# Performance work log

Measured on AMD Instinct MI355X. Metric: run time of the kernel, lower is better.

The kernel has to match this reference:

```python
import jax, jax.numpy as jnp
import numpy as np

DIM = 128
SUPPORT = 1
NL, NM, NG = 5, 20, 100
EPS_BN = 1e-5
EPS_NORM = 1e-12


def knn_idx(vertices, k):
    # vertices: (b, v, 3) -> (b, v, k) indices of k nearest (excluding self)
    sq = jnp.sum(vertices * vertices, axis=-1)  # (b, v)
    dist = -2.0 * jnp.einsum('bic,bjc->bij', vertices, vertices) + sq[:, :, None] + sq[:, None, :]
    _, idx = jax.lax.top_k(-dist, k + 1)  # smallest distances
    return idx[:, :, 1:]


def gather_nbr(t, idx):
    # t: (b, v, c), idx: (b, v, n) -> (b, v, n, c)
    b = t.shape[0]
    return t[jnp.arange(b)[:, None, None], idx]


def conv_layer(idx, vertices, fmap, W, bias, dirs):
    # idx: (b,v,n); fmap: (b,v,DIM); W: (DIM,(S+1)*DIM); bias: ((S+1)*DIM,); dirs: (3,S*DIM)
    nbrs = gather_nbr(vertices, idx)                      # (b,v,n,3)
    d = nbrs - vertices[:, :, None, :]
    d = d / jnp.maximum(jnp.linalg.norm(d, axis=-1, keepdims=True), EPS_NORM)
    sd = dirs / jnp.maximum(jnp.linalg.norm(dirs, axis=0, keepdims=True), EPS_NORM)
    theta = jax.nn.relu(jnp.einsum('bvnc,ck->bvnk', d, sd))  # (b,v,n,S*DIM)
    fo = fmap @ W + bias                                   # (b,v,(S+1)*DIM)
    center = fo[..., :DIM]
    supp = gather_nbr(fo[..., DIM:], idx)                  # (b,v,n,S*DIM)
    b_, v_, n_ = idx.shape
    act = (theta * supp).reshape(b_, v_, n_, SUPPORT, DIM)
    act = jnp.max(act, axis=2).sum(axis=2)                 # max over neighbors, sum over supports
    return center + act                                    # (b,v,DIM)


def bn_relu(x, gamma, beta):
    # training-mode BatchNorm1d over (batch, points) per channel, then ReLU
    mu = jnp.mean(x, axis=(0, 1))
    var = jnp.var(x, axis=(0, 1))
    return jax.nn.relu((x - mu) * jax.lax.rsqrt(var + EPS_BN) * gamma + beta)


def setup_inputs() -> dict:
    key = jax.random.key(0)
    ks = jax.random.split(key, 8)
    B, V = 2, 1024
    return {
        'vertices': jax.random.normal(ks[0], (B, V, 3), jnp.float32),
        'x': jax.random.normal(ks[1], (B, V, DIM), jnp.float32),
        'conv_W': jax.random.normal(ks[2], (6, DIM, (SUPPORT + 1) * DIM), jnp.float32) * 0.05,
        'conv_b': jax.random.normal(ks[3], (6, (SUPPORT + 1) * DIM), jnp.float32) * 0.05,
        'conv_dirs': jax.random.normal(ks[4], (6, 3, SUPPORT * DIM), jnp.float32),
        'bn_gamma': jnp.ones((6, DIM), jnp.float32),
        'bn_beta': jnp.zeros((6, DIM), jnp.float32),
        'down_W': jax.random.normal(ks[5], (3 * DIM, 2 * DIM), jnp.float32) * 0.05,
        'down_b': jax.random.normal(ks[6], (2 * DIM,), jnp.float32) * 0.05,
    }


def reference(vertices, x, conv_W, conv_b, conv_dirs, bn_gamma, bn_beta, down_W, down_b):
    il = knn_idx(vertices, NL)
    im = knn_idx(vertices, NM)
    ig = knn_idx(vertices, NG)
    # param index order: 0=l, 1=m0, 2=m1, 3=g0, 4=g1, 5=g2 (g2 unused, per source bug)
    fl = bn_relu(conv_layer(il, vertices, x, conv_W[0], conv_b[0], conv_dirs[0]), bn_gamma[0], bn_beta[0])
    fm = bn_relu(conv_layer(im, vertices, x, conv_W[1], conv_b[1], conv_dirs[1]), bn_gamma[1], bn_beta[1])
    fm = bn_relu(conv_layer(im, vertices, fm, conv_W[2], conv_b[2], conv_dirs[2]), bn_gamma[2], bn_beta[2])
    fg = bn_relu(conv_layer(ig, vertices, x, conv_W[3], conv_b[3], conv_dirs[3]), bn_gamma[3], bn_beta[3])
    fg = bn_relu(conv_layer(ig, vertices, fg, conv_W[4], conv_b[4], conv_dirs[4]), bn_gamma[4], bn_beta[4])
    # source reuses conv_g0 / bn_g0 for the third global layer
    fg = bn_relu(conv_layer(ig, vertices, fg, conv_W[3], conv_b[3], conv_dirs[3]), bn_gamma[3], bn_beta[3])
    out = jnp.concatenate([fl, fm, fg], axis=2)            # (b, v, 3*DIM)
    return jax.nn.relu(out @ down_W + down_b)              # (b, v, 2*DIM)
```

## Files before the change

### kernel.cpp

```cpp
#include <hip/hip_runtime.h>

__device__ __forceinline__ void do_gemm(
    const float* __restrict__ in, const float* __restrict__ st,
    const float* __restrict__ gm, const float* __restrict__ bt,
    const float* __restrict__ W, const float* __restrict__ bi,
    float* __restrict__ out, int rb, char* smemc)
{
    float* rows  = (float*)smemc;
    float* wch   = rows + 1024;
    float* scale = wch + 4096;
    float* shift = scale + 128;
    int t = threadIdx.x;
    if (t < 128) {
        float sc = 1.0f, sf = 0.0f;
        if (st) {
            float mu  = st[t] * (1.0f/2048.0f);
            float var = st[128+t] * (1.0f/2048.0f) - mu*mu;
            sc = rsqrtf(var + 1e-5f) * gm[t];
            sf = bt[t] - mu*sc;
        }
        scale[t] = sc; shift[t] = sf;
    }
    __syncthreads();
    int r0 = rb * 8;
    {
        float4 v = ((const float4*)(in + r0*128))[t];
        if (st) {
            int c4 = (t & 31) << 2;
            v.x = fmaxf(v.x*scale[c4  ] + shift[c4  ], 0.0f);
            v.y = fmaxf(v.y*scale[c4+1] + shift[c4+1], 0.0f);
            v.z = fmaxf(v.z*scale[c4+2] + shift[c4+2], 0.0f);
            v.w = fmaxf(v.w*scale[c4+3] + shift[c4+3], 0.0f);
        }
        ((float4*)rows)[t] = v;
    }
    int cb = t & 63, rp = (t >> 6) << 1;
    const float* a0r = rows + rp*128;
    const float* a1r = a0r + 128;
    const float4* W4 = (const float4*)W;
    float4* wch4 = (float4*)wch;
    float4 acc0 = make_float4(0.f,0.f,0.f,0.f);
    float4 acc1 = make_float4(0.f,0.f,0.f,0.f);
    for (int c = 0; c < 8; ++c) {
        __syncthreads();
        #pragma unroll
        for (int i = 0; i < 4; ++i)
            wch4[t + 256*i] = W4[c*1024 + t + 256*i];
        __syncthreads();
        int kb = c*16;
        #pragma unroll
        for (int k = 0; k < 16; k += 4) {
            float4 a0 = *(const float4*)(a0r + kb + k);
            float4 a1 = *(const float4*)(a1r + kb + k);
            float4 w;
            w = wch4[(k+0)*64+cb];
            acc0.x += a0.x*w.x; acc0.y += a0.x*w.y; acc0.z += a0.x*w.z; acc0.w += a0.x*w.w;
            acc1.x += a1.x*w.x; acc1.y += a1.x*w.y; acc1.z += a1.x*w.z; acc1.w += a1.x*w.w;
            w = wch4[(k+1)*64+cb];
            acc0.x += a0.y*w.x; acc0.y += a0.y*w.y; acc0.z += a0.y*w.z; acc0.w += a0.y*w.w;
            acc1.x += a1.y*w.x; acc1.y += a1.y*w.y; acc1.z += a1.y*w.z; acc1.w += a1.y*w.w;
            w = wch4[(k+2)*64+cb];
            acc0.x += a0.z*w.x; acc0.y += a0.z*w.y; acc0.z += a0.z*w.z; acc0.w += a0.z*w.w;
            acc1.x += a1.z*w.x; acc1.y += a1.z*w.y; acc1.z += a1.z*w.z; acc1.w += a1.z*w.w;
            w = wch4[(k+3)*64+cb];
            acc0.x += a0.w*w.x; acc0.y += a0.w*w.y; acc0.z += a0.w*w.z; acc0.w += a0.w*w.w;
            acc1.x += a1.w*w.x; acc1.y += a1.w*w.y; acc1.z += a1.w*w.z; acc1.w += a1.w*w.w;
        }
    }
    float4 b4 = ((const float4*)bi)[cb];
    acc0.x += b4.x; acc0.y += b4.y; acc0.z += b4.z; acc0.w += b4.w;
    acc1.x += b4.x; acc1.y += b4.y; acc1.z += b4.z; acc1.w += b4.w;
    ((float4*)out)[(r0+rp  )*64 + cb] = acc0;
    ((float4*)out)[(r0+rp+1)*64 + cb] = acc1;
}

__global__ void k1_kernel(const float* __restrict__ verts, const float* __restrict__ dirs,
                          const float* __restrict__ x,
                          const float* __restrict__ convW, const float* __restrict__ convB,
                          int* __restrict__ idxout, float* __restrict__ sdn,
                          float* __restrict__ st, float* __restrict__ fo)
{
    __shared__ __align__(16) char smem[21504];
    int t = threadIdx.x;
    int blk = blockIdx.x;

    if (blk >= 1280) {
        if (blk == 1286) {
            for (int i = t; i < 768; i += 256) {
                int l = i >> 7, k = i & 127;
                float a = dirs[l*384 + k];
                float b = dirs[l*384 + 128 + k];
                float c = dirs[l*384 + 256 + k];
                float nrm = sqrtf(a*a + b*b + c*c);
                float inv = 1.0f / fmaxf(nrm, 1e-12f);
                sdn[l*384 + k]       = a*inv;
                sdn[l*384 + 128 + k] = b*inv;
                sdn[l*384 + 256 + k] = c*inv;
            }
        } else {
            st[(blk - 1280)*256 + t] = 0.0f;
        }
        return;
    }
    if (blk >= 512) {
        int g = blk - 512;
        int s = g >> 8, rb = g & 255;
        int wi = (s==0) ? 0 : (s==1) ? 1 : 3;
        do_gemm(x, (const float*)0, (const float*)0, (const float*)0,
                convW + wi*32768, convB + wi*256, fo + s*524288, rb, smem);
        return;
    }

    float* xs  = (float*)smem;
    float* ys  = xs + 1024;
    float* zs  = ys + 1024;
    float* sqs = zs + 1024;
    unsigned int* histBase = (unsigned int*)(smem + 16384);
    unsigned int* selBase  = (unsigned int*)(smem + 20480);

    int w = t >> 6, l = t & 63;
    int vglob = blk*4 + w;
    int b = vglob >> 10;
    int v = vglob & 1023;
    unsigned long long* keys = (unsigned long long*)smem + w*256;
    unsigned int* hist = histBase + w*256;
    unsigned int* sel  = selBase + w*4;

    const float* vb = verts + b * 3072;
    for (int i = t; i < 1024; i += 256) {
        float xx = vb[i*3+0], yy = vb[i*3+1], zz = vb[i*3+2];
        xs[i] = xx; ys[i] = yy; zs[i] = zz;
        sqs[i] = xx*xx + yy*yy + zz*zz;
    }
    __syncthreads();

    float cx = xs[v], cy = ys[v], cz = zs[v], csq = sqs[v];
    unsigned long long K16[16];
    #pragma unroll
    for (int q = 0; q < 16; ++q) {
        int j = q*64 + l;
        float dot = cx*xs[j] + cy*ys[j] + cz*zs[j];
        float d = -2.0f*dot + csq + sqs[j];
        unsigned int u = __float_as_uint(d);
        u = (u & 0x80000000u) ? ~u : (u | 0x80000000u);
        K16[q] = (((unsigned long long)u) << 32) | (unsigned long long)j;
    }
    #pragma unroll
    for (int i = 0; i < 4; ++i) hist[l*4 + i] = 0u;
    __syncthreads();

    #pragma unroll
    for (int q = 0; q < 16; ++q)
        atomicAdd(&hist[(unsigned int)(K16[q] >> 56)], 1u);
    __syncthreads();

    {
        unsigned int h0 = hist[l*4], h1 = hist[l*4+1], h2 = hist[l*4+2], h3 = hist[l*4+3];
        unsigned int c1 = h0, c2 = h0+h1, c3 = h0+h1+h2, T = c3+h3;
        unsigned int xacc = T;
        #pragma unroll
        for (int off = 1; off < 64; off <<= 1) {
            unsigned int y = __shfl_up(xacc, off, 64);
            if (l >= off) xacc += y;
        }
        unsigned int P = xacc - T;
        unsigned int ex[4] = {P, P+c1, P+c2, P+c3};
        unsigned int hh[4] = {h0, h1, h2, h3};
        #pragma unroll
        for (int i = 0; i < 4; ++i) {
            if (ex[i] < 101u && ex[i] + hh[i] >= 101u) {
                sel[0] = (unsigned int)(l*4 + i);
                sel[1] = 101u - ex[i];
            }
        }
    }
    __syncthreads();
    unsigned int P8 = sel[0], rank2 = sel[1];
    #pragma unroll
    for (int i = 0; i < 4; ++i) hist[l*4 + i] = 0u;
    __syncthreads();

    #pragma unroll
    for (int q = 0; q < 16; ++q)
        if ((unsigned int)(K16[q] >> 56) == P8)
            atomicAdd(&hist[(unsigned int)(K16[q] >> 48) & 0xFFu], 1u);
    __syncthreads();

    {
        unsigned int h0 = hist[l*4], h1 = hist[l*4+1], h2 = hist[l*4+2], h3 = hist[l*4+3];
        unsigned int c1 = h0, c2 = h0+h1, c3 = h0+h1+h2, T = c3+h3;
        unsigned int xacc = T;
        #pragma unroll
        for (int off = 1; off < 64; off <<= 1) {
            unsigned int y = __shfl_up(xacc, off, 64);
            if (l >= off) xacc += y;
        }
        unsigned int P = xacc - T;
        unsigned int ex[4] = {P, P+c1, P+c2, P+c3};
        unsigned int hh[4] = {h0, h1, h2, h3};
        #pragma unroll
        for (int i = 0; i < 4; ++i) {
            if (ex[i] < rank2 && ex[i] + hh[i] >= rank2) {
                sel[2] = (P8 << 8) | (unsigned int)(l*4 + i);
                sel[3] = 0u;
            }
        }
    }
    __syncthreads();
    unsigned int P16 = sel[2];

    #pragma unroll
    for (int q = 0; q < 16; ++q) {
        if ((unsigned int)(K16[q] >> 48) <= P16) {
            unsigned int pos = atomicAdd(&sel[3], 1u);
            if (pos < 256u) keys[pos] = K16[q];
        }
    }
    __syncthreads();
    unsigned int cnt = sel[3];

    unsigned long long K[4];
    #pragma unroll
    for (int q = 0; q < 4; ++q) {
        unsigned int e = (unsigned int)(l*4 + q);
        K[q] = (e < cnt) ? keys[e] : 0xFFFFFFFFFFFFFFFFULL;
    }

    auto cswap = [&](int qa, int qb, int k) {
        int e = (l << 2) + qa;
        bool up = ((e & k) == 0);
        unsigned long long a = K[qa], bb2 = K[qb];
        unsigned long long mn = a < bb2 ? a : bb2;
        unsigned long long mx = a < bb2 ? bb2 : a;
        K[qa] = up ? mn : mx;
        K[qb] = up ? mx : mn;
    };
    #pragma unroll
    for (int k = 2; k <= 256; k <<= 1) {
        for (int j = k >> 1; j >= 4; j >>= 1) {
            int lj = j >> 2;
            #pragma unroll
            for (int q = 0; q < 4; ++q) {
                unsigned long long other = __shfl_xor(K[q], lj, 64);
                int e = (l << 2) + q;
                bool up = ((e & k) == 0);
                bool lower = ((l & lj) == 0);
                bool takeMin = (lower == up);
                unsigned long long mn = K[q] < other ? K[q] : other;
                unsigned long long mx = K[q] < other ? other : K[q];
                K[q] = takeMin ? mn : mx;
            }
        }
        if (k >= 4) { cswap(0, 2, k); cswap(1, 3, k); }
        cswap(0, 1, k); cswap(2, 3, k);
    }

    #pragma unroll
    for (int q = 0; q < 4; ++q) {
        int e = l*4 + q;
        if (e >= 1 && e <= 100)
            idxout[vglob*100 + (e-1)] = (int)(K[q] & 0xFFFFFFFFu);
    }
}

__global__ void agg_kernel(const int* __restrict__ idx, const float* __restrict__ verts,
                           const float* __restrict__ sdn, const float* __restrict__ fo,
                           int n0, int n1, int n2, int d0, int d1, int d2,
                           float* o0, float* o1, float* o2)
{
    __shared__ float4 ds4s[200];
    __shared__ int jss[200];
    int slot = blockIdx.y;
    int n  = slot==0 ? n0 : slot==1 ? n1 : n2;
    int dI = slot==0 ? d0 : slot==1 ? d1 : d2;
    float* outp = slot==0 ? o0 : slot==1 ? o1 : o2;
    const float* fos = fo + slot * 524288;
    const float* sd = sdn + dI * 384;

    int t = threadIdx.x;
    int h = t >> 7, tt = t & 127;
    float4* ds4 = ds4s + h*100;
    int* js = jss + h*100;
    int r = blockIdx.x*2 + h;
    int b = r >> 10;

    if (tt < n) {
        int j = idx[r*100 + tt];
        js[tt] = j;
        const float* pj = verts + (b*1024 + j)*3;
        const float* pv = verts + r*3;
        float dx = pj[0]-pv[0], dy = pj[1]-pv[1], dz = pj[2]-pv[2];
        float nm = sqrtf(dx*dx + dy*dy + dz*dz);
        float inv = 1.0f / fmaxf(nm, 1e-12f);
        ds4[tt] = make_float4(dx*inv, dy*inv, dz*inv, 0.0f);
    }
    __syncthreads();
    float s0 = sd[tt], s1 = sd[128+tt], s2 = sd[256+tt];
    int bb = b * 1024;
    float m = -3.0e38f;
    for (int q = 0; q < n; q += 5) {
        float th[5];
        const float* p[5];
        #pragma unroll
        for (int u = 0; u < 5; ++u) {
            float4 dq = ds4[q+u];
            th[u] = fmaxf(dq.x*s0 + dq.y*s1 + dq.z*s2, 0.0f);
            p[u] = fos + (size_t)(bb + js[q+u])*256 + 128 + tt;
        }
        float vv[5];
        #pragma unroll
        for (int u = 0; u < 5; ++u) vv[u] = *p[u];
        #pragma unroll
        for (int u = 0; u < 5; ++u) m = fmaxf(m, th[u]*vv[u]);
    }
    outp[r*128 + tt] = fos[r*256 + tt] + m;
}

__global__ void stats_kernel(const float* p0, const float* p1, const float* p2,
                             int i0, int i1, int i2, float* stats)
{
    int slot = blockIdx.y;
    const float* p = slot==0 ? p0 : slot==1 ? p1 : p2;
    float* st = stats + (slot==0 ? i0 : slot==1 ? i1 : i2) * 256;
    __shared__ float s1[256], s2[256];
    int t = threadIdx.x, k = t & 127, half = t >> 7;
    int r0 = blockIdx.x * 128;
    float sum = 0.0f, sq = 0.0f;
    for (int s = 0; s < 64; ++s) {
        float x = p[(r0 + half + 2*s)*128 + k];
        sum += x; sq += x*x;
    }
    s1[t] = sum; s2[t] = sq;
    __syncthreads();
    if (t < 128) {
        atomicAdd(&st[k],     s1[t] + s1[t+128]);
        atomicAdd(&st[128+k], s2[t] + s2[t+128]);
    }
}

__global__ void gemm2_kernel(
    const float* inA, const float* stA, const float* gA, const float* beA,
    const float* WA, const float* biA, float* foA,
    const float* inB, const float* stB, const float* gB, const float* beB,
    const float* WB, const float* biB, float* foB)
{
    __shared__ __align__(16) char smem[21504];
    if (blockIdx.y == 0)
        do_gemm(inA, stA, gA, beA, WA, biA, foA, blockIdx.x, smem);
    else
        do_gemm(inB, stB, gB, beB, WB, biB, foB, blockIdx.x, smem);
}

__global__ void down_kernel(
    const float* __restrict__ p0, const float* __restrict__ st0,
    const float* __restrict__ g0, const float* __restrict__ be0,
    const float* __restrict__ p1, const float* __restrict__ st1,
    const float* __restrict__ g1, const float* __restrict__ be1,
    const float* __restrict__ p2, const float* __restrict__ st2,
    const float* __restrict__ g2, const float* __restrict__ be2,
    const float* __restrict__ dW, const float* __restrict__ db,
    float* __restrict__ out)
{
    __shared__ float rows[8*384];
    __shared__ float wch[16*256];
    __shared__ float scale[384], shift[384];
    int t = threadIdx.x;
    int r0 = blockIdx.x * 8;
    for (int c = t; c < 384; c += 256) {
        int seg = c >> 7, cc = c & 127;
        const float* stp = seg==0 ? st0 : seg==1 ? st1 : st2;
        const float* g   = seg==0 ? g0  : seg==1 ? g1  : g2;
        const float* be  = seg==0 ? be0 : seg==1 ? be1 : be2;
        float mu  = stp[cc] * (1.0f/2048.0f);
        float var = stp[128+cc] * (1.0f/2048.0f) - mu*mu;
        float s = rsqrtf(var + 1e-5f) * g[cc];
        scale[c] = s;
        shift[c] = be[cc] - mu*s;
    }
    __syncthreads();
    for (int q = t; q < 768; q += 256) {
        int row = q / 96, rem = q - row*96;
        int c4 = rem << 2;
        int seg = c4 >> 7, cc = c4 & 127;
        const float* ps = seg==0 ? p0 : seg==1 ? p1 : p2;
        float4 v = *(const float4*)(ps + (r0+row)*128 + cc);
        v.x = fmaxf(v.x*scale[c4  ] + shift[c4  ], 0.0f);
        v.y = fmaxf(v.y*scale[c4+1] + shift[c4+1], 0.0f);
        v.z = fmaxf(v.z*scale[c4+2] + shift[c4+2], 0.0f);
        v.w = fmaxf(v.w*scale[c4+3] + shift[c4+3], 0.0f);
        *(float4*)&rows[row*384 + c4] = v;
    }
    int cb = t & 63, rp = (t >> 6) << 1;
    const float* a0r = rows + rp*384;
    const float* a1r = a0r + 384;
    const float4* W4 = (const float4*)dW;
    float4* wch4 = (float4*)wch;
    float4 acc0 = make_float4(0.f,0.f,0.f,0.f);
    float4 acc1 = make_float4(0.f,0.f,0.f,0.f);
    for (int c = 0; c < 24; ++c) {
        __syncthreads();
        #pragma unroll
        for (int i = 0; i < 4; ++i)
            wch4[t + 256*i] = W4[c*1024 + t + 256*i];
        __syncthreads();
        int kb = c*16;
        #pragma unroll
        for (int k = 0; k < 16; k += 4) {
            float4 a0 = *(const float4*)(a0r + kb + k);
            float4 a1 = *(const float4*)(a1r + kb + k);
            float4 w;
            w = wch4[(k+0)*64+cb];
            acc0.x += a0.x*w.x; acc0.y += a0.x*w.y; acc0.z += a0.x*w.z; acc0.w += a0.x*w.w;
            acc1.x += a1.x*w.x; acc1.y += a1.x*w.y; acc1.z += a1.x*w.z; acc1.w += a1.x*w.w;
            w = wch4[(k+1)*64+cb];
            acc0.x += a0.y*w.x; acc0.y += a0.y*w.y; acc0.z += a0.y*w.z; acc0.w += a0.y*w.w;
            acc1.x += a1.y*w.x; acc1.y += a1.y*w.y; acc1.z += a1.y*w.z; acc1.w += a1.y*w.w;
            w = wch4[(k+2)*64+cb];
            acc0.x += a0.z*w.x; acc0.y += a0.z*w.y; acc0.z += a0.z*w.z; acc0.w += a0.z*w.w;
            acc1.x += a1.z*w.x; acc1.y += a1.z*w.y; acc1.z += a1.z*w.z; acc1.w += a1.z*w.w;
            w = wch4[(k+3)*64+cb];
            acc0.x += a0.w*w.x; acc0.y += a0.w*w.y; acc0.z += a0.w*w.z; acc0.w += a0.w*w.w;
            acc1.x += a1.w*w.x; acc1.y += a1.w*w.y; acc1.z += a1.w*w.z; acc1.w += a1.w*w.w;
        }
    }
    float4 b4 = ((const float4*)db)[cb];
    float4 o0, o1;
    o0.x = fmaxf(acc0.x + b4.x, 0.0f); o0.y = fmaxf(acc0.y + b4.y, 0.0f);
    o0.z = fmaxf(acc0.z + b4.z, 0.0f); o0.w = fmaxf(acc0.w + b4.w, 0.0f);
    o1.x = fmaxf(acc1.x + b4.x, 0.0f); o1.y = fmaxf(acc1.y + b4.y, 0.0f);
    o1.z = fmaxf(acc1.z + b4.z, 0.0f); o1.w = fmaxf(acc1.w + b4.w, 0.0f);
    ((float4*)out)[(r0+rp  )*64 + cb] = o0;
    ((float4*)out)[(r0+rp+1)*64 + cb] = o1;
}

extern "C" void kernel_launch(void* const* d_in, const int* in_sizes, int n_in,
                              void* d_out, int out_size, void* d_ws, size_t ws_size,
                              hipStream_t stream)
{
    (void)in_sizes; (void)n_in; (void)out_size; (void)ws_size;
    const float* verts = (const float*)d_in[0];
    const float* x     = (const float*)d_in[1];
    const float* convW = (const float*)d_in[2];
    const float* convB = (const float*)d_in[3];
    const float* dirs  = (const float*)d_in[4];
    const float* gam   = (const float*)d_in[5];
    const float* bet   = (const float*)d_in[6];
    const float* dW    = (const float*)d_in[7];
    const float* db    = (const float*)d_in[8];
    float* out = (float*)d_out;

    char* ws = (char*)d_ws;
    int*   idxb = (int*)(ws);
    float* sdn  = (float*)(ws + 819200);
    float* st   = (float*)(ws + 828416);
    float* fo   = (float*)(ws + 834560);
    float* p0   = (float*)(ws + 7126016);
    float* p1   = (float*)(ws + 8174592);
    float* p2   = (float*)(ws + 9223168);
    float* p3   = (float*)(ws + 10271744);
    float* p4   = (float*)(ws + 11320320);
    float* p5   = (float*)(ws + 12368896);

    const float* nf = (const float*)0;
    float* nw = (float*)0;
    float* st0 = st,        *st1 = st + 256,  *st2 = st + 512;
    float* st3 = st + 768,  *st4 = st + 1024, *st5 = st + 1280;

    k1_kernel<<<1287, 256, 0, stream>>>(verts, dirs, x, convW, convB,
                                        idxb, sdn, st, fo);
    agg_kernel<<<dim3(1024,3), 256, 0, stream>>>(
        idxb, verts, sdn, fo, 5, 20, 100, 0, 1, 3, p0, p1, p3);
    stats_kernel<<<dim3(16,3), 256, 0, stream>>>(p0, p1, p3, 0, 1, 3, st);
    gemm2_kernel<<<dim3(256,2), 256, 0, stream>>>(
        p1, st1, gam + 128, bet + 128, convW + 65536,  convB + 512,  fo,
        p3, st3, gam + 384, bet + 384, convW + 131072, convB + 1024, fo + 524288);
    agg_kernel<<<dim3(1024,2), 256, 0, stream>>>(
        idxb, verts, sdn, fo, 20, 100, 0, 2, 4, 0, p2, p4, nw);
    stats_kernel<<<dim3(16,2), 256, 0, stream>>>(p2, p4, nf, 2, 4, 0, st);
    gemm2_kernel<<<dim3(256,1), 256, 0, stream>>>(
        p4, st4, gam + 512, bet + 512, convW + 98304, convB + 768, fo,
        nf, nf, nf, nf, nf, nf, nw);
    agg_kernel<<<dim3(1024,1), 256, 0, stream>>>(
        idxb, verts, sdn, fo, 100, 0, 0, 3, 0, 0, p5, nw, nw);
    stats_kernel<<<dim3(16,1), 256, 0, stream>>>(p5, nf, nf, 5, 0, 0, st);
    down_kernel<<<256, 256, 0, stream>>>(
        p0, st0, gam, bet,
        p2, st2, gam + 256, bet + 256,
        p5, st5, gam + 384, bet + 384,
        dW, db, out);
}
```

Baseline: 189.1 us.

## Fuse BatchNorm statistics into aggregation kernel via banked atomics

Removes the separate stats kernel launches by having each aggregation thread atomically add its output value and square into one of 32 banked partial-sum buffers. The consumers (gemm and down kernels) now reduce the 32 banks when computing per-channel mean and variance. k1 zeroes the larger bank region. This saves three launches and a re-read of the activations, at the cost of many global atomics per element and extra reduction loads in the consumers.

```diff
diff --git a/kernel.cpp b/kernel.cpp
--- a/kernel.cpp
+++ b/kernel.cpp
@@ -1,7 +1,8 @@
 #include <hip/hip_runtime.h>
 
+
 __device__ __forceinline__ void do_gemm(
-    const float* __restrict__ in, const float* __restrict__ st,
+    const float* __restrict__ in, const float* __restrict__ stp,
     const float* __restrict__ gm, const float* __restrict__ bt,
     const float* __restrict__ W, const float* __restrict__ bi,
     float* __restrict__ out, int rb, char* smemc)
@@ -13,9 +14,15 @@
     int t = threadIdx.x;
     if (t < 128) {
         float sc = 1.0f, sf = 0.0f;
-        if (st) {
-            float mu  = st[t] * (1.0f/2048.0f);
-            float var = st[128+t] * (1.0f/2048.0f) - mu*mu;
+        if (stp) {
+            float sm = 0.0f, sq = 0.0f;
+            #pragma unroll 8
+            for (int bk = 0; bk < 32; ++bk) {
+                sm += stp[bk*256 + t];
+                sq += stp[bk*256 + 128 + t];
+            }
+            float mu  = sm * (1.0f/2048.0f);
+            float var = sq * (1.0f/2048.0f) - mu*mu;
             sc = rsqrtf(var + 1e-5f) * gm[t];
             sf = bt[t] - mu*sc;
         }
@@ -25,7 +32,7 @@
     int r0 = rb * 8;
     {
         float4 v = ((const float4*)(in + r0*128))[t];
-        if (st) {
+        if (stp) {
             int c4 = (t & 31) << 2;
             v.x = fmaxf(v.x*scale[c4  ] + shift[c4  ], 0.0f);
             v.y = fmaxf(v.y*scale[c4+1] + shift[c4+1], 0.0f);
@@ -78,14 +85,14 @@
                           const float* __restrict__ x,
                           const float* __restrict__ convW, const float* __restrict__ convB,
                           int* __restrict__ idxout, float* __restrict__ sdn,
-                          float* __restrict__ st, float* __restrict__ fo)
+                          float* __restrict__ stp, float* __restrict__ fo)
 {
     __shared__ __align__(16) char smem[21504];
     int t = threadIdx.x;
     int blk = blockIdx.x;
 
     if (blk >= 1280) {
-        if (blk == 1286) {
+        if (blk == 1472) {
             for (int i = t; i < 768; i += 256) {
                 int l = i >> 7, k = i & 127;
                 float a = dirs[l*384 + k];
@@ -98,7 +105,7 @@
                 sdn[l*384 + 256 + k] = c*inv;
             }
         } else {
-            st[(blk - 1280)*256 + t] = 0.0f;
+            stp[(blk - 1280)*256 + t] = 0.0f;
         }
         return;
     }
@@ -266,7 +273,8 @@
 __global__ void agg_kernel(const int* __restrict__ idx, const float* __restrict__ verts,
                            const float* __restrict__ sdn, const float* __restrict__ fo,
                            int n0, int n1, int n2, int d0, int d1, int d2,
-                           float* o0, float* o1, float* o2)
+                           float* o0, float* o1, float* o2,
+                           float* s0p, float* s1p, float* s2p)
 {
     __shared__ float4 ds4s[200];
     __shared__ int jss[200];
@@ -274,6 +282,7 @@
     int n  = slot==0 ? n0 : slot==1 ? n1 : n2;
     int dI = slot==0 ? d0 : slot==1 ? d1 : d2;
     float* outp = slot==0 ? o0 : slot==1 ? o1 : o2;
+    float* stp  = slot==0 ? s0p : slot==1 ? s1p : s2p;
     const float* fos = fo + slot * 524288;
     const float* sd = sdn + dI * 384;
 
@@ -313,29 +322,11 @@
         #pragma unroll
         for (int u = 0; u < 5; ++u) m = fmaxf(m, th[u]*vv[u]);
     }
-    outp[r*128 + tt] = fos[r*256 + tt] + m;
-}
-
-__global__ void stats_kernel(const float* p0, const float* p1, const float* p2,
-                             int i0, int i1, int i2, float* stats)
-{
-    int slot = blockIdx.y;
-    const float* p = slot==0 ? p0 : slot==1 ? p1 : p2;
-    float* st = stats + (slot==0 ? i0 : slot==1 ? i1 : i2) * 256;
-    __shared__ float s1[256], s2[256];
-    int t = threadIdx.x, k = t & 127, half = t >> 7;
-    int r0 = blockIdx.x * 128;
-    float sum = 0.0f, sq = 0.0f;
-    for (int s = 0; s < 64; ++s) {
-        float x = p[(r0 + half + 2*s)*128 + k];
-        sum += x; sq += x*x;
-    }
-    s1[t] = sum; s2[t] = sq;
-    __syncthreads();
-    if (t < 128) {
-        atomicAdd(&st[k],     s1[t] + s1[t+128]);
-        atomicAdd(&st[128+k], s2[t] + s2[t+128]);
-    }
+    float val = fos[r*256 + tt] + m;
+    outp[r*128 + tt] = val;
+    float* bank = stp + (r & 31)*256;
+    atomicAdd(&bank[tt], val);
+    atomicAdd(&bank[128+tt], val*val);
 }
 
 __global__ void gemm2_kernel(
@@ -352,11 +343,11 @@
 }
 
 __global__ void down_kernel(
-    const float* __restrict__ p0, const float* __restrict__ st0,
+    const float* __restrict__ p0, const float* __restrict__ s0p,
     const float* __restrict__ g0, const float* __restrict__ be0,
-    const float* __restrict__ p1, const float* __restrict__ st1,
+    const float* __restrict__ p1, const float* __restrict__ s1p,
     const float* __restrict__ g1, const float* __restrict__ be1,
-    const float* __restrict__ p2, const float* __restrict__ st2,
+    const float* __restrict__ p2, const float* __restrict__ s2p,
     const float* __restrict__ g2, const float* __restrict__ be2,
     const float* __restrict__ dW, const float* __restrict__ db,
     float* __restrict__ out)
@@ -368,11 +359,17 @@
     int r0 = blockIdx.x * 8;
     for (int c = t; c < 384; c += 256) {
         int seg = c >> 7, cc = c & 127;
-        const float* stp = seg==0 ? st0 : seg==1 ? st1 : st2;
+        const float* stp = seg==0 ? s0p : seg==1 ? s1p : s2p;
         const float* g   = seg==0 ? g0  : seg==1 ? g1  : g2;
         const float* be  = seg==0 ? be0 : seg==1 ? be1 : be2;
-        float mu  = stp[cc] * (1.0f/2048.0f);
-        float var = stp[128+cc] * (1.0f/2048.0f) - mu*mu;
+        float sm = 0.0f, sq = 0.0f;
+        #pragma unroll 8
+        for (int bk = 0; bk < 32; ++bk) {
+            sm += stp[bk*256 + cc];
+            sq += stp[bk*256 + 128 + cc];
+        }
+        float mu  = sm * (1.0f/2048.0f);
+        float var = sq * (1.0f/2048.0f) - mu*mu;
         float s = rsqrtf(var + 1e-5f) * g[cc];
         scale[c] = s;
         shift[c] = be[cc] - mu*s;
@@ -452,40 +449,40 @@
     char* ws = (char*)d_ws;
     int*   idxb = (int*)(ws);
     float* sdn  = (float*)(ws + 819200);
-    float* st   = (float*)(ws + 828416);
-    float* fo   = (float*)(ws + 834560);
-    float* p0   = (float*)(ws + 7126016);
-    float* p1   = (float*)(ws + 8174592);
-    float* p2   = (float*)(ws + 9223168);
-    float* p3   = (float*)(ws + 10271744);
-    float* p4   = (float*)(ws + 11320320);
-    float* p5   = (float*)(ws + 12368896);
+    float* stp  = (float*)(ws + 828416);
+    float* fo   = (float*)(ws + 1025024);
+    float* p0   = (float*)(ws + 7316480);
+    float* p1   = (float*)(ws + 8365056);
+    float* p2   = (float*)(ws + 9413632);
+    float* p3   = (float*)(ws + 10462208);
+    float* p4   = (float*)(ws + 11510784);
+    float* p5   = (float*)(ws + 12559360);
 
     const float* nf = (const float*)0;
     float* nw = (float*)0;
-    float* st0 = st,        *st1 = st + 256,  *st2 = st + 512;
-    float* st3 = st + 768,  *st4 = st + 1024, *st5 = st + 1280;
-
-    k1_kernel<<<1287, 256, 0, stream>>>(verts, dirs, x, convW, convB,
-                                        idxb, sdn, st, fo);
+    float* stL0 = stp,         *stL1 = stp + 8192, *stL2 = stp + 16384;
+    float* stL3 = stp + 24576, *stL4 = stp + 32768, *stL5 = stp + 40960;
+
+    k1_kernel<<<1473, 256, 0, stream>>>(verts, dirs, x, convW, convB,
+                                        idxb, sdn, stp, fo);
     agg_kernel<<<dim3(1024,3), 256, 0, stream>>>(
-        idxb, verts, sdn, fo, 5, 20, 100, 0, 1, 3, p0, p1, p3);
-    stats_kernel<<<dim3(16,3), 256, 0, stream>>>(p0, p1, p3, 0, 1, 3, st);
+        idxb, verts, sdn, fo, 5, 20, 100, 0, 1, 3,
+        p0, p1, p3, stL0, stL1, stL3);
     gemm2_kernel<<<dim3(256,2), 256, 0, stream>>>(
-        p1, st1, gam + 128, bet + 128, convW + 65536,  convB + 512,  fo,
-        p3, st3, gam + 384, bet + 384, convW + 131072, convB + 1024, fo + 524288);
+        p1, stL1, gam + 128, bet + 128, convW + 65536,  convB + 512,  fo,
+        p3, stL3, gam + 384, bet + 384, convW + 131072, convB + 1024, fo + 524288);
     agg_kernel<<<dim3(1024,2), 256, 0, stream>>>(
-        idxb, verts, sdn, fo, 20, 100, 0, 2, 4, 0, p2, p4, nw);
-    stats_kernel<<<dim3(16,2), 256, 0, stream>>>(p2, p4, nf, 2, 4, 0, st);
+        idxb, verts, sdn, fo, 20, 100, 0, 2, 4, 0,
+        p2, p4, nw, stL2, stL4, nw);
     gemm2_kernel<<<dim3(256,1), 256, 0, stream>>>(
-        p4, st4, gam + 512, bet + 512, convW + 98304, convB + 768, fo,
+        p4, stL4, gam + 512, bet + 512, convW + 98304, convB + 768, fo,
         nf, nf, nf, nf, nf, nf, nw);
     agg_kernel<<<dim3(1024,1), 256, 0, stream>>>(
-        idxb, verts, sdn, fo, 100, 0, 0, 3, 0, 0, p5, nw, nw);
-    stats_kernel<<<dim3(16,1), 256, 0, stream>>>(p5, nf, nf, 5, 0, 0, st);
+        idxb, verts, sdn, fo, 100, 0, 0, 3, 0, 0,
+        p5, nw, nw, stL5, nw, nw);
     down_kernel<<<256, 256, 0, stream>>>(
-        p0, st0, gam, bet,
-        p2, st2, gam + 256, bet + 256,
-        p5, st5, gam + 384, bet + 384,
+        p0, stL0, gam, bet,
+        p2, stL2, gam + 256, bet + 256,
+        p5, stL5, gam + 384, bet + 384,
         dW, db, out);
 }
```

Result: no change. 187.8 us (-0.7%).
